# Kernel optimization log

Hardware: AMD Instinct MI355X
Metric: run time of the kernel (lower is better)

## Reference

```python
import math
import jax, jax.numpy as jnp
import numpy as np

B, T, C = 2, 2048, 1024
H, D = 16, 64
QC, KC = 128, 256
SCALE = 1.0 / math.sqrt(D)


def _int4_linear(x, w_int8, scale, bias):
    # W = dequant(int8) * per-output-channel scale; y = x @ W.T + bias
    w = w_int8.astype(jnp.float32) * scale[:, None]
    return x @ w.T + bias


def _attention_recompute(q, k, v):
    # q,k,v: (B,H,T,D). Williams-style 2D tiling with streaming (online) softmax, causal.
    nq, nk = T // QC, T // KC
    qt = q.reshape(B, H, nq, QC, D).transpose(2, 0, 1, 3, 4)  # (nq,B,H,QC,D)
    kt = k.reshape(B, H, nk, KC, D).transpose(2, 0, 1, 3, 4)  # (nk,B,H,KC,D)
    vt = v.reshape(B, H, nk, KC, D).transpose(2, 0, 1, 3, 4)
    q_idx = jnp.arange(T).reshape(nq, QC)
    k_idx = jnp.arange(T).reshape(nk, KC)

    def per_qchunk(q_tile, q_pos):
        def step(carry, inp):
            m, l, o = carry
            k_c, v_c, k_pos = inp
            s = jnp.einsum('bhqd,bhkd->bhqk', q_tile, k_c) * SCALE
            mask = k_pos[None, None, None, :] <= q_pos[None, None, :, None]
            s = jnp.where(mask, s, -jnp.inf)
            s_max = jnp.max(s, axis=-1, keepdims=True)
            m_new = jnp.maximum(m, s_max)
            alpha = jnp.exp(m - m_new)
            p = jnp.exp(s - m_new)
            o = o * alpha + jnp.einsum('bhqk,bhkd->bhqd', p, v_c)
            l = l * alpha + jnp.sum(p, axis=-1, keepdims=True)
            return (m_new, l, o), None

        m0 = jnp.full((B, H, QC, 1), -jnp.inf, dtype=q_tile.dtype)
        l0 = jnp.zeros((B, H, QC, 1), dtype=q_tile.dtype)
        o0 = jnp.zeros_like(q_tile)
        (m, l, o), _ = jax.lax.scan(step, (m0, l0, o0), (kt, vt, k_idx))
        return o / (l + 1e-8)

    out = jax.vmap(per_qchunk)(qt, q_idx)  # (nq,B,H,QC,D)
    return out.transpose(1, 2, 0, 3, 4).reshape(B, H, T, D)


def _forward(x, wq, sq, bq, wk, sk, bk, wv, sv, bv, wo, so, bo):
    q = _int4_linear(x, wq, sq, bq).reshape(B, T, H, D).transpose(0, 2, 1, 3)
    k = _int4_linear(x, wk, sk, bk).reshape(B, T, H, D).transpose(0, 2, 1, 3)
    v = _int4_linear(x, wv, sv, bv).reshape(B, T, H, D).transpose(0, 2, 1, 3)
    attn = _attention_recompute(q, k, v)
    y = attn.transpose(0, 2, 1, 3).reshape(B, T, C)
    return _int4_linear(y, wo, so, bo)


def setup_inputs() -> dict:
    key = jax.random.key(0)
    ks = jax.random.split(key, 5)
    x = jax.random.normal(ks[0], (B, T, C), dtype=jnp.float32)

    def w(k):
        return jax.random.randint(k, (C, C), -8, 8, dtype=jnp.int8)

    s = 0.005 * jnp.ones((C,), jnp.float32)  # trainable per-channel scale (init shrunk for sane activations)
    b = jnp.zeros((C,), jnp.float32)
    return {
        'x': x,
        'wq': w(ks[1]), 'sq': s, 'bq': b,
        'wk': w(ks[2]), 'sk': s, 'bk': b,
        'wv': w(ks[3]), 'sv': s, 'bv': b,
        'wo': w(ks[4]), 'so': s, 'bo': b,
    }


def reference(x, wq, sq, bq, wk, sk, bk, wv, sv, bv, wo, so, bo):
    return _forward(x, wq, sq, bq, wk, sk, bk, wv, sv, bv, wo, so, bo)
```

## Files before the change

kernel.cpp:

```cpp
#include <hip/hip_runtime.h>
#include <hip/hip_bf16.h>
#include <stdint.h>

#define BB 2
#define TT 2048
#define CC 1024
#define HH 16
#define DD 64
#define MM (BB*TT)

typedef __bf16 bf16x8 __attribute__((ext_vector_type(8)));
typedef float  f32x4  __attribute__((ext_vector_type(4)));
typedef float  f32x16 __attribute__((ext_vector_type(16)));
typedef unsigned short u16;
typedef unsigned int   u32;

__device__ __forceinline__ u16 f2bf(float f) {
  u32 u = __float_as_uint(f);
  return (u16)((u + 0x7fffu + ((u >> 16) & 1u)) >> 16);
}

__device__ __forceinline__ u32 cvt_pk_bf16(float a, float b) {
  u32 r;
  asm("v_cvt_pk_bf16_f32 %0, %1, %2" : "=v"(r) : "v"(a), "v"(b));
  return r;
}

__device__ __forceinline__ void gload_lds16(const u16* g, u16* l) {
  auto gp = (const u32 __attribute__((address_space(1)))*)(uintptr_t)g;
  auto lp = (u32 __attribute__((address_space(3)))*)(u32)(uintptr_t)l;
  __builtin_amdgcn_global_load_lds(gp, lp, 16, 0, 0);
}

__global__ __launch_bounds__(256)
void k_sentinel(float* __restrict__ out, int n) {
  int i = blockIdx.x * 256 + threadIdx.x;
  if (i < n) out[i] = 9999.0f;
}

__global__ __launch_bounds__(256)
void k_convert(const float* __restrict__ x,
               const int* __restrict__ w0, const int* __restrict__ w1,
               const int* __restrict__ w2, const int* __restrict__ w3,
               u16* __restrict__ xb, u16* __restrict__ wb) {
  const int idx = blockIdx.x * 256 + threadIdx.x;
  const int NX = MM * CC / 4;
  if (idx < NX) {
    float4 v = ((const float4*)x)[idx];
    u32 lo = (u32)f2bf(v.x) | ((u32)f2bf(v.y) << 16);
    u32 hi = (u32)f2bf(v.z) | ((u32)f2bf(v.w) << 16);
    ((uint2*)xb)[idx] = make_uint2(lo, hi);
  } else {
    int u = idx - NX;
    int mat = u >> 18;
    int j = u & 262143;
    const int* ws = (mat == 0) ? w0 : (mat == 1) ? w1 : (mat == 2) ? w2 : w3;
    int4 v = ((const int4*)ws)[j];
    u32 lo = (u32)f2bf((float)v.x) | ((u32)f2bf((float)v.y) << 16);
    u32 hi = (u32)f2bf((float)v.z) | ((u32)f2bf((float)v.w) << 16);
    ((uint2*)wb)[(mat << 18) + j] = make_uint2(lo, hi);
  }
}

__device__ __forceinline__ void gemm_core(const u16* __restrict__ Ag,
                                          const u16* __restrict__ Wg,
                                          int brow, int bcol,
                                          u16* As, u16* Bs, f32x4 acc[4][4]) {
  const int tid  = threadIdx.x;
  const int w    = tid >> 6;
  const int lane = tid & 63;
  const int q = lane & 15, g = lane >> 4;
  const int wm = w >> 1, wn = w & 1;

  for (int kt = 0; kt < CC / 32; ++kt) {
    #pragma unroll
    for (int i = 0; i < 2; ++i) {
      int Lg  = i * 256 + tid;
      int row = Lg >> 2, gc = Lg & 3;
      gload_lds16(Ag + (brow + row) * CC + kt * 32 + gc * 8, As + (i * 256 + w * 64) * 8);
      gload_lds16(Wg + (bcol + row) * CC + kt * 32 + gc * 8, Bs + (i * 256 + w * 64) * 8);
    }
    __syncthreads();
    bf16x8 af[4], bff[4];
    #pragma unroll
    for (int a = 0; a < 4; ++a) af[a]  = *(const bf16x8*)&As[(wm * 64 + a * 16 + q) * 32 + g * 8];
    #pragma unroll
    for (int b = 0; b < 4; ++b) bff[b] = *(const bf16x8*)&Bs[(wn * 64 + b * 16 + q) * 32 + g * 8];
    #pragma unroll
    for (int a = 0; a < 4; ++a) {
      #pragma unroll
      for (int b = 0; b < 4; ++b) {
        acc[a][b] = __builtin_amdgcn_mfma_f32_16x16x32_bf16(af[a], bff[b], acc[a][b], 0, 0, 0);
      }
    }
    __syncthreads();
  }
}

__global__ __launch_bounds__(256)
void k_gemm_qkv(const u16* __restrict__ xb, const u16* __restrict__ wb,
                const float* __restrict__ sq, const float* __restrict__ bq,
                const float* __restrict__ sk, const float* __restrict__ bk,
                const float* __restrict__ sv, const float* __restrict__ bv,
                u16* __restrict__ Qo, u16* __restrict__ Ko, u16* __restrict__ Vt) {
  __shared__ u16 As[128 * 32];
  __shared__ u16 Bs[128 * 32];
  const int bid  = blockIdx.x;
  const int brow = (bid & 31) * 128;
  const int ncol = (bid >> 5) * 128;
  const int mat  = ncol >> 10;
  const int bcol = ncol & 1023;
  const u16* W = wb + (mat << 20);

  f32x4 acc[4][4];
  #pragma unroll
  for (int a = 0; a < 4; ++a)
    #pragma unroll
    for (int b = 0; b < 4; ++b) { f32x4 z = {0.f, 0.f, 0.f, 0.f}; acc[a][b] = z; }

  gemm_core(xb, W, brow, bcol, As, Bs, acc);

  const int tid = threadIdx.x;
  const int w = tid >> 6, lane = tid & 63;
  const int q = lane & 15, g = lane >> 4;
  const int wm = w >> 1, wn = w & 1;
  const float* sarr = (mat == 0) ? sq : (mat == 1) ? sk : sv;
  const float* barr = (mat == 0) ? bq : (mat == 1) ? bk : bv;

  #pragma unroll
  for (int bt = 0; bt < 4; ++bt) {
    const int c = bcol + wn * 64 + bt * 16 + q;
    const float sc = sarr[c];
    const float bi = barr[c];
    const int h = c >> 6, d = c & 63;
    #pragma unroll
    for (int a = 0; a < 4; ++a) {
      #pragma unroll
      for (int r = 0; r < 4; ++r) {
        const int m = brow + wm * 64 + a * 16 + 4 * g + r;
        const int b_ = m >> 11, t = m & 2047;
        const u16 val = f2bf(acc[a][bt][r] * sc + bi);
        if (mat == 0)      Qo[(((size_t)(b_ * HH + h) * TT) + t) * DD + d] = val;
        else if (mat == 1) Ko[(((size_t)(b_ * HH + h) * TT) + t) * DD + d] = val;
        else               Vt[((size_t)(b_ * HH + h) * DD + d) * TT + t] = val;
      }
    }
  }
}

__global__ __launch_bounds__(256, 2)
void k_attn(const u16* __restrict__ Q, const u16* __restrict__ K,
            const u16* __restrict__ Vt, u16* __restrict__ Y) {
  __shared__ u16 kbuf[2][2][64 * 64];
  __shared__ u16 vbuf[2][2][64 * 64];
  const int tid = threadIdx.x;
  const int w = tid >> 6, lane = tid & 63;
  const int q = lane & 31, hi = lane >> 5;
  const int r = w >> 1, u_ = w & 1;
  const int bid = blockIdx.x;
  const int bh = bid & 31;
  const int j  = (bid >> 5) & 7;
  const int qt = bid >> 8;
  const int v  = (qt == 0) ? (31 - j) : (qt == 1) ? (16 + j)
               : (qt == 2) ? (15 - j) : j;
  const int qw = v * 64 + 32 * r;
  const int qg = qw + q;
  const u16* Qh = Q  + (size_t)bh * TT * DD;
  const u16* Kh = K  + (size_t)bh * TT * DD;
  const u16* Vh = Vt + (size_t)bh * DD * TT;
  const int b_ = bh >> 4, h = bh & 15;
  constexpr float SE = 0.125f * 1.44269504088896340736f;

  bf16x8 qf[4];
  #pragma unroll
  for (int c = 0; c < 4; ++c)
    qf[c] = *(const bf16x8*)&Qh[(qw + q) * DD + 16 * c + 8 * hi];

  f32x16 oacc[2];
  oacc[0] = f32x16{}; oacc[1] = f32x16{};
  float m_run = -1.0e30f;
  float l_vec[8];
  #pragma unroll
  for (int u2 = 0; u2 < 8; ++u2) l_vec[u2] = 0.f;

  const int nkb = v + 1;
  const int P = (nkb + 1) >> 1;

  #define STAGE(BUFI, PH)                                                           \
    {                                                                               \
      int kbA = min(128 * (PH), TT - 64);                                           \
      int kbB = min(128 * (PH) + 64, TT - 64);                                      \
      _Pragma("unroll")                                                             \
      for (int jj = 0; jj < 2; ++jj) {                                              \
        int kbase_j = jj ? kbB : kbA;                                               \
        _Pragma("unroll")                                                           \
        for (int r2 = 0; r2 < 2; ++r2) {                                            \
          int g = r2 * 256 + tid;                                                   \
          int row = g >> 3, cB = (g & 7) << 4;                                      \
          int scB = cB ^ ((row & 7) << 4);                                          \
          gload_lds16(Kh + (size_t)(kbase_j + row) * DD + (scB >> 1),               \
                      &kbuf[BUFI][jj][(r2 * 256 + w * 64) * 8]);                    \
        }                                                                           \
        _Pragma("unroll")                                                           \
        for (int r2 = 0; r2 < 2; ++r2) {                                            \
          int g = r2 * 256 + tid;                                                   \
          int row = g >> 3, cB = (g & 7) << 4;                                      \
          int scB = cB ^ ((row & 7) << 4);                                          \
          gload_lds16(Vh + (size_t)row * TT + kbase_j + (scB >> 1),                 \
                      &vbuf[BUFI][jj][(r2 * 256 + w * 64) * 8]);                    \
        }                                                                           \
      }                                                                             \
    }

  STAGE(0, 0);
  for (int i = 0; i < P; ++i) {
    asm volatile("s_waitcnt vmcnt(0)" ::: "memory");
    __builtin_amdgcn_s_barrier();
    __builtin_amdgcn_sched_barrier(0);
    if (i + 1 < P) STAGE((i + 1) & 1, i + 1);

    const int kb2 = 2 * i + u_;
    if (kb2 < nkb) {
      const int kbase = kb2 * 64;
      const u16* kl = kbuf[i & 1][u_];
      const u16* vl = vbuf[i & 1][u_];

      bf16x8 kf[2][4];
      #pragma unroll
      for (int s = 0; s < 2; ++s)
        #pragma unroll
        for (int c = 0; c < 4; ++c) {
          const int row = 32 * s + q, cB = 32 * c + 16 * hi;
          kf[s][c] = *(const bf16x8*)&kl[(row * 128 + (cB ^ ((row & 7) << 4))) >> 1];
        }
      f32x16 sacc[2];
      sacc[0] = f32x16{}; sacc[1] = f32x16{};
      __builtin_amdgcn_s_setprio(1);
      #pragma unroll
      for (int c = 0; c < 4; ++c) {
        sacc[0] = __builtin_amdgcn_mfma_f32_32x32x16_bf16(kf[0][c], qf[c], sacc[0], 0, 0, 0);
        sacc[1] = __builtin_amdgcn_mfma_f32_32x32x16_bf16(kf[1][c], qf[c], sacc[1], 0, 0, 0);
      }
      __builtin_amdgcn_s_setprio(0);

      bf16x8 vf[2][2][2];
      #pragma unroll
      for (int dt = 0; dt < 2; ++dt)
        #pragma unroll
        for (int s = 0; s < 2; ++s)
          #pragma unroll
          for (int c2 = 0; c2 < 2; ++c2) {
            const int row = dt * 32 + q, cB = 64 * s + 32 * c2 + 16 * hi;
            vf[dt][s][c2] = *(const bf16x8*)&vl[(row * 128 + (cB ^ ((row & 7) << 4))) >> 1];
          }

      float sr[32];
      #pragma unroll
      for (int s = 0; s < 2; ++s)
        #pragma unroll
        for (int rr = 0; rr < 16; ++rr) sr[s * 16 + rr] = sacc[s][rr];
      if (kbase + 63 > qw) {
        #pragma unroll
        for (int s = 0; s < 2; ++s)
          #pragma unroll
          for (int rr = 0; rr < 16; ++rr)
            if (kbase + 32 * s + (rr & 3) + 8 * (rr >> 2) + 4 * hi > qg)
              sr[s * 16 + rr] = -__builtin_inff();
      }
      float mx[16];
      #pragma unroll
      for (int u2 = 0; u2 < 16; ++u2) mx[u2] = fmaxf(sr[u2], sr[u2 + 16]);
      #pragma unroll
      for (int st = 8; st > 0; st >>= 1)
        #pragma unroll
        for (int u2 = 0; u2 < st; ++u2) mx[u2] = fmaxf(mx[u2], mx[u2 + st]);
      const float pmax = fmaxf(mx[0], __shfl_xor(mx[0], 32)) * SE;
      const bool keep = __all(pmax <= m_run + 8.0f);
      const float m_new = keep ? m_run : fmaxf(m_run, pmax);
      const float nm = -m_new;
      float p[32];
      #pragma unroll
      for (int u2 = 0; u2 < 32; ++u2)
        p[u2] = __builtin_amdgcn_exp2f(fmaf(sr[u2], SE, nm));
      if (!keep) {
        const float alpha = __builtin_amdgcn_exp2f(m_run - m_new);
        m_run = m_new;
        oacc[0] *= alpha;
        oacc[1] *= alpha;
        #pragma unroll
        for (int u2 = 0; u2 < 8; ++u2) l_vec[u2] *= alpha;
      }
      float t16[16];
      #pragma unroll
      for (int u2 = 0; u2 < 16; ++u2) t16[u2] = p[u2] + p[u2 + 16];
      #pragma unroll
      for (int u2 = 0; u2 < 8; ++u2) l_vec[u2] += t16[u2] + t16[u2 + 8];

      u32 Aw[8], Bw[8];
      #pragma unroll
      for (int n = 0; n < 8; ++n) {
        const int base = ((n >> 2) * 16) + ((n & 3) << 2);
        Aw[n] = cvt_pk_bf16(p[base + 0], p[base + 1]);
        Bw[n] = cvt_pk_bf16(p[base + 2], p[base + 3]);
      }
      bf16x8 pf[2][2];
      #pragma unroll
      for (int s = 0; s < 2; ++s)
        #pragma unroll
        for (int c2 = 0; c2 < 2; ++c2) {
          const int n0 = 4 * s + 2 * c2;
          u32 x0 = Aw[n0], x2 = Aw[n0 + 1];
          asm volatile("v_permlane32_swap_b32 %0, %1" : "+v"(x0), "+v"(x2));
          u32 x1 = Bw[n0], x3 = Bw[n0 + 1];
          asm volatile("v_permlane32_swap_b32 %0, %1" : "+v"(x1), "+v"(x3));
          union { u32 uw[4]; bf16x8 vv; } U;
          U.uw[0] = x0; U.uw[1] = x1; U.uw[2] = x2; U.uw[3] = x3;
          pf[s][c2] = U.vv;
        }

      __builtin_amdgcn_s_setprio(1);
      #pragma unroll
      for (int s = 0; s < 2; ++s)
        #pragma unroll
        for (int c2 = 0; c2 < 2; ++c2) {
          oacc[0] = __builtin_amdgcn_mfma_f32_32x32x16_bf16(vf[0][s][c2], pf[s][c2], oacc[0], 0, 0, 0);
          oacc[1] = __builtin_amdgcn_mfma_f32_32x32x16_bf16(vf[1][s][c2], pf[s][c2], oacc[1], 0, 0, 0);
        }
      __builtin_amdgcn_s_setprio(0);
    }
  }
  #undef STAGE

  __syncthreads();
  float l_run = ((l_vec[0] + l_vec[1]) + (l_vec[2] + l_vec[3]))
              + ((l_vec[4] + l_vec[5]) + (l_vec[6] + l_vec[7]));
  float* ms = ((float*)kbuf) + (r * 64 + lane) * 37;
  if (u_ == 1) {
    #pragma unroll
    for (int dt = 0; dt < 2; ++dt)
      #pragma unroll
      for (int e = 0; e < 16; ++e) ms[dt * 16 + e] = oacc[dt][e];
    ms[32] = m_run;
    ms[33] = l_run;
  }
  __syncthreads();
  if (u_ == 0) {
    const float m1 = ms[32], l1 = ms[33];
    const float mt = fmaxf(m_run, m1);
    const float s0 = __builtin_amdgcn_exp2f(m_run - mt);
    const float s1 = __builtin_amdgcn_exp2f(m1 - mt);
    float lt = l_run * s0 + l1 * s1;
    lt += __shfl_xor(lt, 32);
    const float inv = 1.f / (lt + 1e-8f);
    #pragma unroll
    for (int dt = 0; dt < 2; ++dt)
      #pragma unroll
      for (int n = 0; n < 4; ++n) {
        const float o0 = (oacc[dt][4 * n + 0] * s0 + ms[dt * 16 + 4 * n + 0] * s1) * inv;
        const float o1 = (oacc[dt][4 * n + 1] * s0 + ms[dt * 16 + 4 * n + 1] * s1) * inv;
        const float o2 = (oacc[dt][4 * n + 2] * s0 + ms[dt * 16 + 4 * n + 2] * s1) * inv;
        const float o3 = (oacc[dt][4 * n + 3] * s0 + ms[dt * 16 + 4 * n + 3] * s1) * inv;
        u32 lo  = cvt_pk_bf16(o0, o1);
        u32 hi2 = cvt_pk_bf16(o2, o3);
        *(uint2*)&Y[(size_t)(b_ * TT + qg) * CC + h * 64 + 32 * dt + 8 * n + 4 * hi]
          = make_uint2(lo, hi2);
      }
  }
}

__global__ __launch_bounds__(256)
void k_gemm_o(const u16* __restrict__ Yb, const u16* __restrict__ Wo,
              const float* __restrict__ so, const float* __restrict__ bo,
              float* __restrict__ out) {
  __shared__ u16 As[128 * 32];
  __shared__ u16 Bs[128 * 32];
  const int bid = blockIdx.x;
  const int brow = (bid & 31) * 128;
  const int bcol = (bid >> 5) * 128;
  f32x4 acc[4][4];
  #pragma unroll
  for (int a = 0; a < 4; ++a)
    #pragma unroll
    for (int b = 0; b < 4; ++b) { f32x4 z = {0.f, 0.f, 0.f, 0.f}; acc[a][b] = z; }

  gemm_core(Yb, Wo, brow, bcol, As, Bs, acc);

  const int tid = threadIdx.x;
  const int w = tid >> 6, lane = tid & 63;
  const int q = lane & 15, g = lane >> 4;
  const int wm = w >> 1, wn = w & 1;
  #pragma unroll
  for (int bt = 0; bt < 4; ++bt) {
    const int c = bcol + wn * 64 + bt * 16 + q;
    const float sc = so[c], bi = bo[c];
    #pragma unroll
    for (int a = 0; a < 4; ++a) {
      const int mbase = brow + wm * 64 + a * 16 + 4 * g;
      #pragma unroll
      for (int r = 0; r < 4; ++r) {
        out[(size_t)(mbase + r) * CC + c] = acc[a][bt][r] * sc + bi;
      }
    }
  }
}

extern "C" void kernel_launch(void* const* d_in, const int* in_sizes, int n_in,
                              void* d_out, int out_size, void* d_ws, size_t ws_size,
                              hipStream_t stream) {
  const float* x  = (const float*)d_in[0];
  const int*   wq = (const int*)d_in[1];
  const float* sq = (const float*)d_in[2];
  const float* bq = (const float*)d_in[3];
  const int*   wk = (const int*)d_in[4];
  const float* sk = (const float*)d_in[5];
  const float* bk = (const float*)d_in[6];
  const int*   wv = (const int*)d_in[7];
  const float* sv = (const float*)d_in[8];
  const float* bv = (const float*)d_in[9];
  const int*   wo = (const int*)d_in[10];
  const float* so = (const float*)d_in[11];
  const float* bo = (const float*)d_in[12];

  const size_t NEED = (40u << 20);
  if (ws_size < NEED) {
    k_sentinel<<<dim3((out_size + 255) / 256), dim3(256), 0, stream>>>((float*)d_out, out_size);
    return;
  }

  char* ws = (char*)d_ws;
  u16* xb = (u16*)(ws);
  u16* wb = (u16*)(ws + (8u  << 20));
  u16* Qb = (u16*)(ws + (16u << 20));
  u16* Kb = (u16*)(ws + (24u << 20));
  u16* Vt = (u16*)(ws + (32u << 20));
  u16* Yb = xb;

  k_convert <<<dim3(8192), dim3(256), 0, stream>>>(x, wq, wk, wv, wo, xb, wb);
  k_gemm_qkv<<<dim3(768),  dim3(256), 0, stream>>>(xb, wb, sq, bq, sk, bk, sv, bv, Qb, Kb, Vt);
  k_attn    <<<dim3(1024), dim3(256), 0, stream>>>(Qb, Kb, Vt, Yb);
  k_gemm_o  <<<dim3(256),  dim3(256), 0, stream>>>(Yb, wb + (3u << 20), so, bo, (float*)d_out);
}
```

Before: 108.9 us.

## Double-buffer GEMM LDS tiles and stage V-transpose stores through shared memory

The GEMM core now uses two LDS buffers, so the global-to-LDS load of the next K tile is issued right after the barrier and overlaps the MFMAs on the current tile. This leaves one barrier per iteration instead of two, and the MFMA block runs at raised wave priority. The V projection epilogue now writes its transposed output through an LDS staging tile, so each global store is a coalesced 16-byte write along T instead of a scattered 2-byte write. The cost is twice the shared memory per GEMM block and extra barriers in the V epilogue.

```diff
diff --git a/kernel.cpp b/kernel.cpp
--- a/kernel.cpp
+++ b/kernel.cpp
@@ -65,27 +65,41 @@
 __device__ __forceinline__ void gemm_core(const u16* __restrict__ Ag,
                                           const u16* __restrict__ Wg,
                                           int brow, int bcol,
-                                          u16* As, u16* Bs, f32x4 acc[4][4]) {
+                                          u16* sh, f32x4 acc[4][4]) {
   const int tid  = threadIdx.x;
   const int w    = tid >> 6;
   const int lane = tid & 63;
   const int q = lane & 15, g = lane >> 4;
   const int wm = w >> 1, wn = w & 1;
 
+#define GSTAGE(BUF, KT)                                                         \
+    {                                                                           \
+      _Pragma("unroll")                                                         \
+      for (int i2 = 0; i2 < 2; ++i2) {                                          \
+        int Lg = i2 * 256 + tid;                                                \
+        int row = Lg >> 2, gc = Lg & 3;                                         \
+        gload_lds16(Ag + (size_t)(brow + row) * CC + (KT) * 32 + gc * 8,        \
+                    sh + (BUF) * 4096 + (i2 * 256 + w * 64) * 8);               \
+        gload_lds16(Wg + (size_t)(bcol + row) * CC + (KT) * 32 + gc * 8,        \
+                    sh + 8192 + (BUF) * 4096 + (i2 * 256 + w * 64) * 8);        \
+      }                                                                         \
+    }
+
+  GSTAGE(0, 0);
   for (int kt = 0; kt < CC / 32; ++kt) {
-    #pragma unroll
-    for (int i = 0; i < 2; ++i) {
-      int Lg  = i * 256 + tid;
-      int row = Lg >> 2, gc = Lg & 3;
-      gload_lds16(Ag + (brow + row) * CC + kt * 32 + gc * 8, As + (i * 256 + w * 64) * 8);
-      gload_lds16(Wg + (bcol + row) * CC + kt * 32 + gc * 8, Bs + (i * 256 + w * 64) * 8);
-    }
-    __syncthreads();
+    asm volatile("s_waitcnt vmcnt(0)" ::: "memory");
+    __builtin_amdgcn_s_barrier();
+    __builtin_amdgcn_sched_barrier(0);
+    if (kt + 1 < CC / 32) GSTAGE((kt + 1) & 1, kt + 1);
+
+    const u16* Asb = sh + (kt & 1) * 4096;
+    const u16* Bsb = sh + 8192 + (kt & 1) * 4096;
     bf16x8 af[4], bff[4];
     #pragma unroll
-    for (int a = 0; a < 4; ++a) af[a]  = *(const bf16x8*)&As[(wm * 64 + a * 16 + q) * 32 + g * 8];
-    #pragma unroll
-    for (int b = 0; b < 4; ++b) bff[b] = *(const bf16x8*)&Bs[(wn * 64 + b * 16 + q) * 32 + g * 8];
+    for (int a = 0; a < 4; ++a) af[a]  = *(const bf16x8*)&Asb[(wm * 64 + a * 16 + q) * 32 + g * 8];
+    #pragma unroll
+    for (int b = 0; b < 4; ++b) bff[b] = *(const bf16x8*)&Bsb[(wn * 64 + b * 16 + q) * 32 + g * 8];
+    __builtin_amdgcn_s_setprio(1);
     #pragma unroll
     for (int a = 0; a < 4; ++a) {
       #pragma unroll
@@ -93,8 +107,9 @@
         acc[a][b] = __builtin_amdgcn_mfma_f32_16x16x32_bf16(af[a], bff[b], acc[a][b], 0, 0, 0);
       }
     }
-    __syncthreads();
-  }
+    __builtin_amdgcn_s_setprio(0);
+  }
+#undef GSTAGE
 }
 
 __global__ __launch_bounds__(256)
@@ -103,8 +118,7 @@
                 const float* __restrict__ sk, const float* __restrict__ bk,
                 const float* __restrict__ sv, const float* __restrict__ bv,
                 u16* __restrict__ Qo, u16* __restrict__ Ko, u16* __restrict__ Vt) {
-  __shared__ u16 As[128 * 32];
-  __shared__ u16 Bs[128 * 32];
+  __shared__ u16 sh[4][4096];
   const int bid  = blockIdx.x;
   const int brow = (bid & 31) * 128;
   const int ncol = (bid >> 5) * 128;
@@ -118,7 +132,7 @@
     #pragma unroll
     for (int b = 0; b < 4; ++b) { f32x4 z = {0.f, 0.f, 0.f, 0.f}; acc[a][b] = z; }
 
-  gemm_core(xb, W, brow, bcol, As, Bs, acc);
+  gemm_core(xb, W, brow, bcol, &sh[0][0], acc);
 
   const int tid = threadIdx.x;
   const int w = tid >> 6, lane = tid & 63;
@@ -127,23 +141,54 @@
   const float* sarr = (mat == 0) ? sq : (mat == 1) ? sk : sv;
   const float* barr = (mat == 0) ? bq : (mat == 1) ? bk : bv;
 
-  #pragma unroll
-  for (int bt = 0; bt < 4; ++bt) {
-    const int c = bcol + wn * 64 + bt * 16 + q;
-    const float sc = sarr[c];
-    const float bi = barr[c];
-    const int h = c >> 6, d = c & 63;
-    #pragma unroll
-    for (int a = 0; a < 4; ++a) {
-      #pragma unroll
-      for (int r = 0; r < 4; ++r) {
-        const int m = brow + wm * 64 + a * 16 + 4 * g + r;
-        const int b_ = m >> 11, t = m & 2047;
-        const u16 val = f2bf(acc[a][bt][r] * sc + bi);
-        if (mat == 0)      Qo[(((size_t)(b_ * HH + h) * TT) + t) * DD + d] = val;
-        else if (mat == 1) Ko[(((size_t)(b_ * HH + h) * TT) + t) * DD + d] = val;
-        else               Vt[((size_t)(b_ * HH + h) * DD + d) * TT + t] = val;
-      }
+  if (mat < 2) {
+    u16* Out = (mat == 0) ? Qo : Ko;
+    #pragma unroll
+    for (int bt = 0; bt < 4; ++bt) {
+      const int c = bcol + wn * 64 + bt * 16 + q;
+      const float sc = sarr[c];
+      const float bi = barr[c];
+      const int h = c >> 6, d = c & 63;
+      #pragma unroll
+      for (int a = 0; a < 4; ++a) {
+        #pragma unroll
+        for (int r = 0; r < 4; ++r) {
+          const int m = brow + wm * 64 + a * 16 + 4 * g + r;
+          const int b_ = m >> 11, t = m & 2047;
+          Out[(((size_t)(b_ * HH + h) * TT) + t) * DD + d] = f2bf(acc[a][bt][r] * sc + bi);
+        }
+      }
+    }
+  } else {
+    __syncthreads();
+    u16* lt = &sh[0][0];
+    const int b_ = brow >> 11, t0 = brow & 2047;
+    #pragma unroll
+    for (int hh = 0; hh < 2; ++hh) {
+      if (wn == hh) {
+        #pragma unroll
+        for (int bt = 0; bt < 4; ++bt) {
+          const int c = bcol + wn * 64 + bt * 16 + q;
+          const float sc = sarr[c];
+          const float bi = barr[c];
+          #pragma unroll
+          for (int a = 0; a < 4; ++a) {
+            u32 lo  = cvt_pk_bf16(acc[a][bt][0] * sc + bi, acc[a][bt][1] * sc + bi);
+            u32 hi2 = cvt_pk_bf16(acc[a][bt][2] * sc + bi, acc[a][bt][3] * sc + bi);
+            *(uint2*)&lt[(bt * 16 + q) * 136 + wm * 64 + a * 16 + 4 * g] = make_uint2(lo, hi2);
+          }
+        }
+      }
+      __syncthreads();
+      {
+        const int d = tid >> 2, seg = tid & 3;
+        const int hg = (bcol >> 6) + hh;
+        const size_t base = ((size_t)(b_ * HH + hg) * DD + d) * TT + t0 + seg * 32;
+        #pragma unroll
+        for (int j2 = 0; j2 < 4; ++j2)
+          *(uint4*)&Vt[base + j2 * 8] = *(const uint4*)&lt[d * 136 + seg * 32 + j2 * 8];
+      }
+      __syncthreads();
     }
   }
 }
@@ -372,8 +417,7 @@
 void k_gemm_o(const u16* __restrict__ Yb, const u16* __restrict__ Wo,
               const float* __restrict__ so, const float* __restrict__ bo,
               float* __restrict__ out) {
-  __shared__ u16 As[128 * 32];
-  __shared__ u16 Bs[128 * 32];
+  __shared__ u16 sh[4][4096];
   const int bid = blockIdx.x;
   const int brow = (bid & 31) * 128;
   const int bcol = (bid >> 5) * 128;
@@ -383,7 +427,7 @@
     #pragma unroll
     for (int b = 0; b < 4; ++b) { f32x4 z = {0.f, 0.f, 0.f, 0.f}; acc[a][b] = z; }
 
-  gemm_core(Yb, Wo, brow, bcol, As, Bs, acc);
+  gemm_core(Yb, Wo, brow, bcol, &sh[0][0], acc);
 
   const int tid = threadIdx.x;
   const int w = tid >> 6, lane = tid & 63;
```

Result: slower. 111.4 us (+2.3%).
